# Kernel optimization log

Measured on AMD Instinct MI355X. Metric: run time of the kernel, lower is better.

## Reference

```python
import jax, jax.numpy as jnp
import numpy as np
from jax import lax

SUR_BETA = 4.0
THRESH = 1.0
ALPHA = float(np.exp(-1.0 / 20.0))  # membrane decay, tau_mem=20
BETA = float(np.exp(-1.0 / 5.0))    # synaptic decay, tau_syn=5

@jax.custom_vjp
def spike(x):
    return (x >= 0).astype(jnp.float32)

def _spike_fwd(x):
    return spike(x), x

def _spike_bwd(x, g):
    e = jnp.exp(-SUR_BETA * jnp.abs(x))
    sg = SUR_BETA * e / (2.0 * (1.0 + e) ** 2)
    return (g * sg,)

spike.defvjp(_spike_fwd, _spike_bwd)

def lif_layer(x, W, b):
    # x: [B, T, Din] -> spikes [B, T, H]
    xt = jnp.einsum('bti,ih->bth', x, W) + b
    B, T, H = xt.shape
    z = jnp.zeros((B, H), xt.dtype)
    def step(carry, x_t):
        v, i = carry
        i = BETA * i + x_t
        v = ALPHA * v + i
        s = spike(v - THRESH)
        v = v * (1.0 - s)  # multiplicative reset
        return (v, i), s
    _, sp = lax.scan(step, (z, z), xt.transpose(1, 0, 2))
    return sp.transpose(1, 0, 2)

def layer_norm(x, scale, bias, eps=1e-6):
    m = jnp.mean(x, axis=-1, keepdims=True)
    v = jnp.mean((x - m) ** 2, axis=-1, keepdims=True)
    return (x - m) / jnp.sqrt(v + eps) * scale + bias

def setup_inputs() -> dict:
    key = jax.random.key(0)
    ks = jax.random.split(key, 6)
    B, T, S, F = 64, 512, 64, 16
    D = S * F  # 1024
    def w(k, shape, fan):
        return (jax.random.normal(k, shape, jnp.float32) / np.sqrt(fan)).astype(jnp.float32)
    return dict(
        spike_trains=(jax.random.uniform(ks[0], (B, T, S, F)) < 0.2).astype(jnp.float32),
        W0=w(ks[1], (D, 256), D), b0=jnp.zeros((256,), jnp.float32),
        W1=w(ks[2], (256, 128), 256), b1=jnp.zeros((128,), jnp.float32),
        W2=w(ks[3], (128, 64), 128), b2=jnp.zeros((64,), jnp.float32),
        ln1_scale=jnp.ones((256,), jnp.float32), ln1_bias=jnp.zeros((256,), jnp.float32),
        ln2_scale=jnp.ones((128,), jnp.float32), ln2_bias=jnp.zeros((128,), jnp.float32),
        Wc=w(ks[4], (B, 2), B), bc=jnp.zeros((2,), jnp.float32),
    )

def reference(spike_trains, W0, b0, W1, b1, W2, b2,
              ln1_scale, ln1_bias, ln2_scale, ln2_bias, Wc, bc):
    B, T, S, F = spike_trains.shape
    x = spike_trains.reshape(B, T, S * F)
    x = lif_layer(x, W0, b0)                                   # [B,T,256]
    x = lif_layer(layer_norm(x, ln1_scale, ln1_bias), W1, b1)  # [B,T,128]
    x = lif_layer(layer_norm(x, ln2_scale, ln2_bias), W2, b2)  # [B,T,64]
    pooled = jnp.mean(x, axis=(1, 2))  # [B]  (faithful to source: mean over time AND hidden)
    logits = pooled @ Wc + bc          # [num_classes] -- classifier sees batch as feature dim
    return (logits, pooled, jnp.mean(x))
```

## Files before the change

### kernel.cpp

```cpp
#include <hip/hip_runtime.h>

#define T_STEPS 512
#define BATCH 64

__device__ constexpr float ALPHA_ = 0.95122942450071400910f;
__device__ constexpr float BETA_  = 0.81873075307798185867f;

typedef __attribute__((ext_vector_type(8))) short bf16x8;
typedef __attribute__((ext_vector_type(4))) float f32x4;

__device__ inline unsigned short f2bf_rne(float f) {
  union { float f; unsigned int u; } v{f};
  const unsigned int u = v.u;
  return (unsigned short)((u + 0x7FFFu + ((u >> 16) & 1u)) >> 16);
}
__device__ inline float bf2f(unsigned short h) {
  union { unsigned int u; float f; } v{(unsigned int)h << 16};
  return v.f;
}

__device__ inline void gload16(const void* g, void* l) {
  __builtin_amdgcn_global_load_lds(
      (const __attribute__((address_space(1))) unsigned int*)g,
      (__attribute__((address_space(3))) unsigned int*)l, 16, 0, 0);
}

__device__ inline unsigned int pkbf(float first, float second) {
#if __has_builtin(__builtin_amdgcn_perm)
  return __builtin_amdgcn_perm(__float_as_uint(second), __float_as_uint(first),
                               0x07060302u);
#else
  return (__float_as_uint(first) >> 16) | (__float_as_uint(second) & 0xFFFF0000u);
#endif
}

__device__ inline bf16x8 cvt_frag(const f32x4 lo, const f32x4 hi) {
  union { unsigned int w[4]; bf16x8 v; } u;
  u.w[0] = pkbf(lo.x, lo.y);
  u.w[1] = pkbf(lo.z, lo.w);
  u.w[2] = pkbf(hi.x, hi.y);
  u.w[3] = pkbf(hi.z, hi.w);
  return u.v;
}

template <int WM, int WC, int TM, bool A_F32, bool LNFOLD>
__global__ __launch_bounds__(256) void gemm_pipe(
    const void* __restrict__ Av, const char* __restrict__ Bhi,
    const char* __restrict__ Blo, const float* __restrict__ uvec,
    const float* __restrict__ cvec, float* __restrict__ C, int N, int K) {
  constexpr int BM = WM * TM;
  constexpr int BN = WC * 64;
  constexpr int FM = TM / 16;
  constexpr int ABY = BM * 64;
  constexpr int BBY = BN * 64;
  constexpr int BUFBY = ABY + 2 * BBY;
  __shared__ char smem[2 * BUFBY];

  const int tid = threadIdx.x;
  const int lane = tid & 63;
  const int wave = tid >> 6;
  const int wm = wave / WC, wc = wave % WC;
  const int l15 = lane & 15, l4 = lane >> 4;
  const int row0 = blockIdx.y * BM;
  const int col0 = blockIdx.x * BN;
  const int KB = K / 32;

  const char* Ab = (const char*)Av;

  const float* ap0 = nullptr;
  const float* ap1 = nullptr;
  int au0 = 0, au1 = 0;
  if constexpr (A_F32) {
    const int r0 = tid >> 2, j0 = tid & 3;
    ap0 = (const float*)Ab + (size_t)(row0 + r0) * K + j0 * 8;
    ap1 = ap0 + (size_t)64 * K;
    au0 = ((r0 >> 4) << 6) + (j0 << 4) + (r0 & 15);
    au1 = au0 + 256;
  }

  f32x4 acc[FM][4] = {};
  f32x4 acc1[FM] = {};
  const bf16x8 ONES = {0x3F80, 0x3F80, 0x3F80, 0x3F80,
                       0x3F80, 0x3F80, 0x3F80, 0x3F80};

  f32x4 a0, a1, a2, a3;

  {
    char* Abuf = smem;
    char* Bh = smem + ABY;
    char* Bl = Bh + BBY;
    if constexpr (A_F32) {
      a0 = *(const f32x4*)(ap0);
      a1 = *(const f32x4*)(ap0 + 4);
      a2 = *(const f32x4*)(ap1);
      a3 = *(const f32x4*)(ap1 + 4);
    } else {
#pragma unroll
      for (int i = 0; i < BM / 64; ++i) {
        const int unit = i * 256 + tid;
        const int r = ((unit >> 6) << 4) | (unit & 15);
        const int j = (unit >> 4) & 3;
        gload16(Ab + ((size_t)(row0 + r) * K + j * 8) * 2, Abuf + unit * 16);
      }
    }
#pragma unroll
    for (int g = 0; g < WC; ++g) {
      const size_t so = (((size_t)(blockIdx.x * WC + g) * KB) * 256 + tid) * 16;
      gload16(Bhi + so, Bh + (g * 256 + tid) * 16);
      gload16(Blo + so, Bl + (g * 256 + tid) * 16);
    }
    if constexpr (A_F32) {
      *(bf16x8*)(Abuf + au0 * 16) = cvt_frag(a0, a1);
      *(bf16x8*)(Abuf + au1 * 16) = cvt_frag(a2, a3);
    }
    __syncthreads();
  }

  int cur = 0;
  for (int kb = 0; kb < KB; ++kb) {
    char* bufc = smem + cur * BUFBY;
    char* bufn = smem + (cur ^ 1) * BUFBY;
    const bool pf = (kb + 1 < KB);

    if (pf) {
      if constexpr (A_F32) {
        const float* p0 = ap0 + (size_t)(kb + 1) * 32;
        const float* p1 = ap1 + (size_t)(kb + 1) * 32;
        a0 = *(const f32x4*)p0;
        a1 = *(const f32x4*)(p0 + 4);
        a2 = *(const f32x4*)p1;
        a3 = *(const f32x4*)(p1 + 4);
      } else {
#pragma unroll
        for (int i = 0; i < BM / 64; ++i) {
          const int unit = i * 256 + tid;
          const int r = ((unit >> 6) << 4) | (unit & 15);
          const int j = (unit >> 4) & 3;
          gload16(Ab + ((size_t)(row0 + r) * K + (kb + 1) * 32 + j * 8) * 2,
                  bufn + unit * 16);
        }
      }
#pragma unroll
      for (int g = 0; g < WC; ++g) {
        const size_t so =
            (((size_t)(blockIdx.x * WC + g) * KB + (kb + 1)) * 256 + tid) * 16;
        gload16(Bhi + so, bufn + ABY + (g * 256 + tid) * 16);
        gload16(Blo + so, bufn + ABY + BBY + (g * 256 + tid) * 16);
      }
    }

    bf16x8 af[FM], bh[4], bl[4];
#pragma unroll
    for (int m = 0; m < FM; ++m)
      af[m] = *(const bf16x8*)(bufc + ((wm * FM + m) * 64 + lane) * 16);
#pragma unroll
    for (int n = 0; n < 4; ++n) {
      bh[n] = *(const bf16x8*)(bufc + ABY + (wc * 256 + n * 64 + lane) * 16);
      bl[n] = *(const bf16x8*)(bufc + ABY + BBY + (wc * 256 + n * 64 + lane) * 16);
    }

#pragma unroll
    for (int m = 0; m < FM; ++m) {
#pragma unroll
      for (int n = 0; n < 4; ++n) {
        acc[m][n] = __builtin_amdgcn_mfma_f32_16x16x32_bf16(af[m], bh[n], acc[m][n], 0, 0, 0);
        acc[m][n] = __builtin_amdgcn_mfma_f32_16x16x32_bf16(af[m], bl[n], acc[m][n], 0, 0, 0);
      }
      if constexpr (LNFOLD)
        acc1[m] = __builtin_amdgcn_mfma_f32_16x16x32_bf16(af[m], ONES, acc1[m], 0, 0, 0);
    }

    if (pf && A_F32) {
      *(bf16x8*)(bufn + au0 * 16) = cvt_frag(a0, a1);
      *(bf16x8*)(bufn + au1 * 16) = cvt_frag(a2, a3);
    }
    __syncthreads();
    cur ^= 1;
  }

  const int row0w = row0 + wm * TM;
  const int col0w = col0 + wc * 64;
#pragma unroll
  for (int m = 0; m < FM; ++m) {
    const int rbase = row0w + m * 16 + l4 * 4;
    float iv[4], mv[4];
    if constexpr (LNFOLD) {
#pragma unroll
      for (int r = 0; r < 4; ++r) {
        const float mean = acc1[m][r] / (float)K;
        const float inv = 1.0f / sqrtf(mean * (1.f - mean) + 1e-6f);
        iv[r] = inv;
        mv[r] = mean * inv;
      }
    }
#pragma unroll
    for (int n = 0; n < 4; ++n) {
      const int c = col0w + n * 16 + l15;
      const float cc = cvec[c];
      float uu = 0.f;
      if constexpr (LNFOLD) uu = uvec[c];
#pragma unroll
      for (int r = 0; r < 4; ++r) {
        float v;
        if constexpr (LNFOLD) v = iv[r] * acc[m][n][r] - mv[r] * uu + cc;
        else v = acc[m][n][r] + cc;
        C[(size_t)(rbase + r) * N + c] = v;
      }
    }
  }
}

__global__ void prep_split(const float* __restrict__ W, const float* __restrict__ s,
                           char* __restrict__ hi, char* __restrict__ lo,
                           int K, int N) {
  const int g = blockIdx.x * 256 + threadIdx.x;
  const int total = (K * N) / 8;
  if (g >= total) return;
  constexpr int UB = 256;
  const int KB = K / 32;
  const int unit = g % UB;
  const int kb = (g / UB) % KB;
  const int cb = g / (UB * KB);
  const int n = cb * 64 + ((unit >> 6) << 4) + (unit & 15);
  const int kbase = kb * 32 + ((unit >> 4) & 3) * 8;
  short h8[8], l8[8];
#pragma unroll
  for (int jj = 0; jj < 8; ++jj) {
    const int k = kbase + jj;
    float w = W[(size_t)k * N + n];
    if (s) w *= s[k];
    const unsigned short hb = f2bf_rne(w);
    const unsigned short lb = f2bf_rne(w - bf2f(hb));
    h8[jj] = (short)hb;
    l8[jj] = (short)lb;
  }
  *(bf16x8*)(hi + (size_t)g * 16) = *(const bf16x8*)h8;
  *(bf16x8*)(lo + (size_t)g * 16) = *(const bf16x8*)l8;
}

__global__ __launch_bounds__(256) void prep_consts(
    const float* __restrict__ W, const float* __restrict__ s,
    const float* __restrict__ b, const float* __restrict__ bias2,
    float* __restrict__ u, float* __restrict__ c, int K, int N) {
  const int n = blockIdx.x;
  const int t = threadIdx.x;
  float us = 0.f, cs = 0.f;
  for (int k = t; k < K; k += 256) {
    const float w = W[(size_t)k * N + n];
    us += s[k] * w;
    cs += b[k] * w;
  }
  __shared__ float su[256], sc[256];
  su[t] = us;
  sc[t] = cs;
  __syncthreads();
  for (int o = 128; o > 0; o >>= 1) {
    if (t < o) { su[t] += su[t + o]; sc[t] += sc[t + o]; }
    __syncthreads();
  }
  if (t == 0) { u[n] = su[0]; c[n] = sc[0] + bias2[n]; }
}

template <int H, bool SPIKE_OUT, bool ACCUM>
__global__ void lif_scan(const float* __restrict__ xt,
                         unsigned short* __restrict__ sp,
                         float* __restrict__ tsum) {
  const int n = blockIdx.x * 64 + threadIdx.x;
  const int b = n / H, h = n % H;
  const float* p = xt + (size_t)b * T_STEPS * H + h;
  unsigned short* q = nullptr;
  if constexpr (SPIKE_OUT) q = sp + (size_t)b * T_STEPS * H + h;

  float v = 0.f, cur = 0.f, ts = 0.f;
  for (int t = 0; t < T_STEPS; t += 16) {
    float x[16];
#pragma unroll
    for (int u = 0; u < 16; ++u) x[u] = p[(size_t)u * H];
#pragma unroll
    for (int u = 0; u < 16; ++u) {
      cur = BETA_ * cur + x[u];
      v = ALPHA_ * v + cur;
      const bool sb = (v >= 1.f);
      if constexpr (SPIKE_OUT) q[(size_t)u * H] = sb ? 0x3F80 : 0;
      if constexpr (ACCUM) ts += sb ? 1.f : 0.f;
      v = sb ? 0.f : v;
    }
    p += (size_t)16 * H;
    if constexpr (SPIKE_OUT) q += (size_t)16 * H;
  }
  if constexpr (ACCUM) tsum[n] = ts;
}

__global__ void finalize(const float* __restrict__ tsum,
                         const float* __restrict__ Wc,
                         const float* __restrict__ bc,
                         float* __restrict__ out) {
  const int b = threadIdx.x;
  float s = 0.f;
#pragma unroll 8
  for (int h = 0; h < 64; ++h) s += tsum[b * 64 + h];
  const float pooled = s * (1.0f / (512.f * 64.f));
  out[2 + b] = pooled;

  float tot = pooled;
  float l0 = pooled * Wc[b * 2 + 0];
  float l1 = pooled * Wc[b * 2 + 1];
#pragma unroll
  for (int off = 32; off > 0; off >>= 1) {
    tot += __shfl_xor(tot, off);
    l0 += __shfl_xor(l0, off);
    l1 += __shfl_xor(l1, off);
  }
  if (b == 0) {
    out[0] = l0 + bc[0];
    out[1] = l1 + bc[1];
    out[66] = tot * (1.0f / 64.f);
  }
}

extern "C" void kernel_launch(void* const* d_in, const int* in_sizes, int n_in,
                              void* d_out, int out_size, void* d_ws, size_t ws_size,
                              hipStream_t stream) {
  const float* X    = (const float*)d_in[0];
  const float* W0   = (const float*)d_in[1];
  const float* b0   = (const float*)d_in[2];
  const float* W1   = (const float*)d_in[3];
  const float* b1   = (const float*)d_in[4];
  const float* W2   = (const float*)d_in[5];
  const float* b2   = (const float*)d_in[6];
  const float* ln1s = (const float*)d_in[7];
  const float* ln1b = (const float*)d_in[8];
  const float* ln2s = (const float*)d_in[9];
  const float* ln2b = (const float*)d_in[10];
  const float* Wc   = (const float*)d_in[11];
  const float* bc   = (const float*)d_in[12];
  float* out = (float*)d_out;

  char* w = (char*)d_ws;
  float* buf0 = (float*)w;
  float* buf1 = (float*)w;
  float* buf2 = (float*)(w + 16777216);
  size_t off = 33554432;
  unsigned short* sp0 = (unsigned short*)(w + off); off += 16777216;
  unsigned short* sp1 = (unsigned short*)(w + off); off += 8388608;
  char* hi0 = w + off; off += 524288;
  char* lo0 = w + off; off += 524288;
  char* hi1 = w + off; off += 65536;
  char* lo1 = w + off; off += 65536;
  char* hi2 = w + off; off += 16384;
  char* lo2 = w + off; off += 16384;
  float* u1 = (float*)(w + off); off += 512;
  float* c1 = (float*)(w + off); off += 512;
  float* u2 = (float*)(w + off); off += 256;
  float* c2 = (float*)(w + off); off += 256;
  float* tsum = (float*)(w + off); off += 16384;

  const int M = 32768;

  prep_split<<<128, 256, 0, stream>>>(W0, nullptr, hi0, lo0, 1024, 256);
  prep_split<<<16, 256, 0, stream>>>(W1, ln1s, hi1, lo1, 256, 128);
  prep_split<<<4, 256, 0, stream>>>(W2, ln2s, hi2, lo2, 128, 64);
  prep_consts<<<128, 256, 0, stream>>>(W1, ln1s, ln1b, b1, u1, c1, 256, 128);
  prep_consts<<<64, 256, 0, stream>>>(W2, ln2s, ln2b, b2, u2, c2, 128, 64);

  gemm_pipe<2, 2, 64, true, false><<<dim3(2, M / 128), 256, 0, stream>>>(
      X, hi0, lo0, nullptr, b0, buf0, 256, 1024);
  lif_scan<256, true, false><<<(BATCH * 256) / 64, 64, 0, stream>>>(buf0, sp0, nullptr);

  gemm_pipe<4, 1, 32, false, true><<<dim3(2, M / 128), 256, 0, stream>>>(
      sp0, hi1, lo1, u1, c1, buf1, 128, 256);
  lif_scan<128, true, false><<<(BATCH * 128) / 64, 64, 0, stream>>>(buf1, sp1, nullptr);

  gemm_pipe<4, 1, 32, false, true><<<dim3(1, M / 128), 256, 0, stream>>>(
      sp1, hi2, lo2, u2, c2, buf2, 64, 128);
  lif_scan<64, false, true><<<(BATCH * 64) / 64, 64, 0, stream>>>(buf2, nullptr, tsum);

  finalize<<<1, 64, 0, stream>>>(tsum, Wc, bc, out);
}
```

Before: 141.2 us.

## Stage fp32 A tiles via async LDS loads and convert at fragment read

The GEMM now loads fp32 A tiles directly into LDS with async global_load_lds instead of staging them through registers and converting before an LDS store. The bf16 conversion moves to fragment-read time. Source pointers are precomputed once, and the loop syncs with an explicit vmcnt wait plus barrier. The LIF scan loop unroll grows from 16 to 32 timesteps to allow more loads in flight. In exchange, the fp32 A tile doubles LDS footprint, which may lower occupancy, and every wave repeats the conversion work per fragment.

```diff
diff --git a/kernel.cpp b/kernel.cpp
--- a/kernel.cpp
+++ b/kernel.cpp
@@ -51,9 +51,10 @@
   constexpr int BM = WM * TM;
   constexpr int BN = WC * 64;
   constexpr int FM = TM / 16;
-  constexpr int ABY = BM * 64;
-  constexpr int BBY = BN * 64;
-  constexpr int BUFBY = ABY + 2 * BBY;
+  constexpr int ABY = A_F32 ? BM * 128 : BM * 64;
+  constexpr int BBH = BN * 64;
+  constexpr int BUFBY = ABY + 2 * BBH;
+  constexpr int API = (ABY / 16) / 256;
   __shared__ char smem[2 * BUFBY];
 
   const int tid = threadIdx.x;
@@ -67,96 +68,72 @@
 
   const char* Ab = (const char*)Av;
 
-  const float* ap0 = nullptr;
-  const float* ap1 = nullptr;
-  int au0 = 0, au1 = 0;
-  if constexpr (A_F32) {
-    const int r0 = tid >> 2, j0 = tid & 3;
-    ap0 = (const float*)Ab + (size_t)(row0 + r0) * K + j0 * 8;
-    ap1 = ap0 + (size_t)64 * K;
-    au0 = ((r0 >> 4) << 6) + (j0 << 4) + (r0 & 15);
-    au1 = au0 + 256;
-  }
+  const char* a_src[API];
+#pragma unroll
+  for (int i = 0; i < API; ++i) {
+    const int unit = i * 256 + tid;
+    if constexpr (A_F32) {
+      const int fr = unit >> 7, h = (unit >> 6) & 1, ln = unit & 63;
+      a_src[i] = Ab + ((size_t)(row0 + fr * 16 + (ln & 15)) * K + ((ln >> 4) * 8)) * 4 + h * 16;
+    } else {
+      const int r = ((unit >> 6) << 4) | (unit & 15);
+      const int j = (unit >> 4) & 3;
+      a_src[i] = Ab + ((size_t)(row0 + r) * K + j * 8) * 2;
+    }
+  }
+  const char* bh_src[WC];
+  const char* bl_src[WC];
+#pragma unroll
+  for (int g = 0; g < WC; ++g) {
+    const size_t so = ((size_t)(blockIdx.x * WC + g) * KB) * 4096 + (size_t)tid * 16;
+    bh_src[g] = Bhi + so;
+    bl_src[g] = Blo + so;
+  }
+
+  auto stage = [&](int kb, char* buf) {
+#pragma unroll
+    for (int i = 0; i < API; ++i) {
+      const int unit = i * 256 + tid;
+      gload16(a_src[i] + (size_t)kb * (A_F32 ? 128 : 64), buf + unit * 16);
+    }
+#pragma unroll
+    for (int g = 0; g < WC; ++g) {
+      gload16(bh_src[g] + (size_t)kb * 4096, buf + ABY + (g * 256 + tid) * 16);
+      gload16(bl_src[g] + (size_t)kb * 4096, buf + ABY + BBH + (g * 256 + tid) * 16);
+    }
+  };
 
   f32x4 acc[FM][4] = {};
   f32x4 acc1[FM] = {};
   const bf16x8 ONES = {0x3F80, 0x3F80, 0x3F80, 0x3F80,
                        0x3F80, 0x3F80, 0x3F80, 0x3F80};
 
-  f32x4 a0, a1, a2, a3;
-
-  {
-    char* Abuf = smem;
-    char* Bh = smem + ABY;
-    char* Bl = Bh + BBY;
-    if constexpr (A_F32) {
-      a0 = *(const f32x4*)(ap0);
-      a1 = *(const f32x4*)(ap0 + 4);
-      a2 = *(const f32x4*)(ap1);
-      a3 = *(const f32x4*)(ap1 + 4);
-    } else {
-#pragma unroll
-      for (int i = 0; i < BM / 64; ++i) {
-        const int unit = i * 256 + tid;
-        const int r = ((unit >> 6) << 4) | (unit & 15);
-        const int j = (unit >> 4) & 3;
-        gload16(Ab + ((size_t)(row0 + r) * K + j * 8) * 2, Abuf + unit * 16);
+  stage(0, smem);
+  asm volatile("s_waitcnt vmcnt(0)" ::: "memory");
+  __builtin_amdgcn_s_barrier();
+  __builtin_amdgcn_sched_barrier(0);
+
+  for (int kb = 0; kb < KB; ++kb) {
+    char* bufc = smem + (kb & 1) * BUFBY;
+    char* bufn = smem + ((kb & 1) ^ 1) * BUFBY;
+    if (kb + 1 < KB) stage(kb + 1, bufn);
+
+    bf16x8 af[FM], bh[4], bl[4];
+#pragma unroll
+    for (int m = 0; m < FM; ++m) {
+      const int fr = wm * FM + m;
+      if constexpr (A_F32) {
+        const f32x4 lo = *(const f32x4*)(bufc + ((fr * 2 + 0) * 64 + lane) * 16);
+        const f32x4 hi = *(const f32x4*)(bufc + ((fr * 2 + 1) * 64 + lane) * 16);
+        af[m] = cvt_frag(lo, hi);
+      } else {
+        af[m] = *(const bf16x8*)(bufc + (fr * 64 + lane) * 16);
       }
     }
-#pragma unroll
-    for (int g = 0; g < WC; ++g) {
-      const size_t so = (((size_t)(blockIdx.x * WC + g) * KB) * 256 + tid) * 16;
-      gload16(Bhi + so, Bh + (g * 256 + tid) * 16);
-      gload16(Blo + so, Bl + (g * 256 + tid) * 16);
-    }
-    if constexpr (A_F32) {
-      *(bf16x8*)(Abuf + au0 * 16) = cvt_frag(a0, a1);
-      *(bf16x8*)(Abuf + au1 * 16) = cvt_frag(a2, a3);
-    }
-    __syncthreads();
-  }
-
-  int cur = 0;
-  for (int kb = 0; kb < KB; ++kb) {
-    char* bufc = smem + cur * BUFBY;
-    char* bufn = smem + (cur ^ 1) * BUFBY;
-    const bool pf = (kb + 1 < KB);
-
-    if (pf) {
-      if constexpr (A_F32) {
-        const float* p0 = ap0 + (size_t)(kb + 1) * 32;
-        const float* p1 = ap1 + (size_t)(kb + 1) * 32;
-        a0 = *(const f32x4*)p0;
-        a1 = *(const f32x4*)(p0 + 4);
-        a2 = *(const f32x4*)p1;
-        a3 = *(const f32x4*)(p1 + 4);
-      } else {
-#pragma unroll
-        for (int i = 0; i < BM / 64; ++i) {
-          const int unit = i * 256 + tid;
-          const int r = ((unit >> 6) << 4) | (unit & 15);
-          const int j = (unit >> 4) & 3;
-          gload16(Ab + ((size_t)(row0 + r) * K + (kb + 1) * 32 + j * 8) * 2,
-                  bufn + unit * 16);
-        }
-      }
-#pragma unroll
-      for (int g = 0; g < WC; ++g) {
-        const size_t so =
-            (((size_t)(blockIdx.x * WC + g) * KB + (kb + 1)) * 256 + tid) * 16;
-        gload16(Bhi + so, bufn + ABY + (g * 256 + tid) * 16);
-        gload16(Blo + so, bufn + ABY + BBY + (g * 256 + tid) * 16);
-      }
-    }
-
-    bf16x8 af[FM], bh[4], bl[4];
-#pragma unroll
-    for (int m = 0; m < FM; ++m)
-      af[m] = *(const bf16x8*)(bufc + ((wm * FM + m) * 64 + lane) * 16);
 #pragma unroll
     for (int n = 0; n < 4; ++n) {
       bh[n] = *(const bf16x8*)(bufc + ABY + (wc * 256 + n * 64 + lane) * 16);
-      bl[n] = *(const bf16x8*)(bufc + ABY + BBY + (wc * 256 + n * 64 + lane) * 16);
+      bl[n] = *(const bf16x8*)(bufc + ABY + BBH + (wc * 256 + n * 64 + lane) * 16);
     }
 
 #pragma unroll
@@ -170,12 +147,9 @@
         acc1[m] = __builtin_amdgcn_mfma_f32_16x16x32_bf16(af[m], ONES, acc1[m], 0, 0, 0);
     }
 
-    if (pf && A_F32) {
-      *(bf16x8*)(bufn + au0 * 16) = cvt_frag(a0, a1);
-      *(bf16x8*)(bufn + au1 * 16) = cvt_frag(a2, a3);
-    }
-    __syncthreads();
-    cur ^= 1;
+    asm volatile("s_waitcnt vmcnt(0)" ::: "memory");
+    __builtin_amdgcn_s_barrier();
+    __builtin_amdgcn_sched_barrier(0);
   }
 
   const int row0w = row0 + wm * TM;
@@ -272,12 +246,12 @@
   if constexpr (SPIKE_OUT) q = sp + (size_t)b * T_STEPS * H + h;
 
   float v = 0.f, cur = 0.f, ts = 0.f;
-  for (int t = 0; t < T_STEPS; t += 16) {
-    float x[16];
-#pragma unroll
-    for (int u = 0; u < 16; ++u) x[u] = p[(size_t)u * H];
-#pragma unroll
-    for (int u = 0; u < 16; ++u) {
+  for (int t = 0; t < T_STEPS; t += 32) {
+    float x[32];
+#pragma unroll
+    for (int u = 0; u < 32; ++u) x[u] = p[(size_t)u * H];
+#pragma unroll
+    for (int u = 0; u < 32; ++u) {
       cur = BETA_ * cur + x[u];
       v = ALPHA_ * v + cur;
       const bool sb = (v >= 1.f);
@@ -285,8 +259,8 @@
       if constexpr (ACCUM) ts += sb ? 1.f : 0.f;
       v = sb ? 0.f : v;
     }
-    p += (size_t)16 * H;
-    if constexpr (SPIKE_OUT) q += (size_t)16 * H;
+    p += (size_t)32 * H;
+    if constexpr (SPIKE_OUT) q += (size_t)32 * H;
   }
   if constexpr (ACCUM) tsum[n] = ts;
 }
```

Result: faster. 135.4 us (-4.1%).
